# Kernel optimization log

Measured on AMD Instinct MI355X. Metric: run time of the kernel, lower is better.

The kernel has to match this reference:

```python
import jax, jax.numpy as jnp
import numpy as np

B, S, E, H = 2, 2048, 1024, 16
D = E // H  # head_dim = 64

def setup_inputs() -> dict:
    key = jax.random.key(0)
    ks = jax.random.split(key, 5)
    scale = 0.02
    return {
        "x": jax.random.normal(ks[0], (B, S, E), dtype=jnp.float32),
        "Wq": jax.random.normal(ks[1], (E, E), dtype=jnp.float32) * scale,
        "Wk": jax.random.normal(ks[2], (E, E), dtype=jnp.float32) * scale,
        "Wv": jax.random.normal(ks[3], (E, E), dtype=jnp.float32) * scale,
        "Wo": jax.random.normal(ks[4], (E, E), dtype=jnp.float32) * scale,
        "bo": jnp.zeros((E,), dtype=jnp.float32),
    }

def reference(x, Wq, Wk, Wv, Wo, bo):
    b, s, e = x.shape
    # Linear projections (torch Linear: x @ W.T), split heads -> (b, h, s, d)
    q = (x @ Wq.T).reshape(b, s, H, D).transpose(0, 2, 1, 3)
    k = (x @ Wk.T).reshape(b, s, H, D).transpose(0, 2, 1, 3)
    v = (x @ Wv.T).reshape(b, s, H, D).transpose(0, 2, 1, 3)
    # Full materialized causal scores (b, h, s, s)
    scores = jnp.einsum("bhqd,bhkd->bhqk", q, k)
    causal = jnp.tril(jnp.ones((s, s), dtype=bool))  # True = keep
    scores = jnp.where(causal, scores, -jnp.inf)
    attn = jax.nn.softmax(scores / jnp.sqrt(jnp.float32(D)), axis=-1)
    ctx = jnp.einsum("bhqk,bhkd->bhqd", attn, v)
    ctx = ctx.transpose(0, 2, 1, 3).reshape(b, s, e)
    return ctx @ Wo.T + bo
```

## Files before the change

kernel.cpp:

```cpp
#include <hip/hip_runtime.h>
#include <hip/hip_bf16.h>

typedef __attribute__((ext_vector_type(8))) short short8_t;
typedef __attribute__((ext_vector_type(4))) short s4v;
typedef __attribute__((ext_vector_type(4))) float f32x4_t;
typedef __attribute__((ext_vector_type(4))) unsigned u32x4_t;
using u16 = unsigned short;

constexpr int S_LEN = 2048;
constexpr int EMB   = 1024;
constexpr int NH    = 16;
constexpr int HD    = 64;
constexpr int BATCH = 2;
constexpr int MR    = BATCH * S_LEN;
constexpr int E3    = 3 * EMB;

#define L2E 1.44269504f

__device__ __forceinline__ u16 f2bf(float f) {
  unsigned u = __builtin_bit_cast(unsigned, f);
  unsigned r = 0x7fffu + ((u >> 16) & 1u);
  return (u16)((u + r) >> 16);
}

__device__ __forceinline__ unsigned pkbf(float a, float b) {
  __hip_bfloat162 h = __float22bfloat162_rn(make_float2(a, b));
  unsigned u;
  __builtin_memcpy(&u, &h, 4);
  return u;
}

__device__ __forceinline__ void gld16(const void* g, void* l) {
  __builtin_amdgcn_global_load_lds(
      (const __attribute__((address_space(1))) void*)g,
      (__attribute__((address_space(3))) void*)l, 16, 0, 0);
}

template <int OFF>
__device__ __forceinline__ s4v tr16(const __attribute__((address_space(3))) u16* p) {
  s4v d;
  asm volatile("ds_read_b64_tr_b16 %0, %1 offset:%2"
               : "=v"(d) : "v"(p), "n"(OFF));
  return d;
}

__global__ void k_cvt_all(const float* __restrict__ x, const float* __restrict__ Wq,
                          const float* __restrict__ Wk, const float* __restrict__ Wv,
                          const float* __restrict__ Wo, u16* __restrict__ out) {
  int i = blockIdx.x * 256 + threadIdx.x;
  const float* src;
  int j;
  float sc = 1.0f;
  if (i < (1 << 20)) {
    src = x; j = i;
  } else {
    int jj = i - (1 << 20);
    int r = jj >> 18;
    j = jj & ((1 << 18) - 1);
    src = (r == 0) ? Wq : (r == 1) ? Wk : (r == 2) ? Wv : Wo;
    if (r == 0) sc = 0.125f;
  }
  float4 v = reinterpret_cast<const float4*>(src)[j];
  ushort4 o;
  o.x = f2bf(v.x * sc); o.y = f2bf(v.y * sc);
  o.z = f2bf(v.z * sc); o.w = f2bf(v.w * sc);
  reinterpret_cast<ushort4*>(out)[i] = o;
}

__global__ __launch_bounds__(512, 1) void k_gemm256(
    const u16* __restrict__ A, const u16* __restrict__ Bw,
    u16* __restrict__ C, int M, int N) {
  constexpr int K = 1024;
  __shared__ u16 Ab[2][16384];
  __shared__ u16 Bb[2][16384];

  const int t    = threadIdx.x;
  const int ww   = t >> 6;
  const int l    = t & 63;
  const int ln15 = t & 15;
  const int lg   = (t >> 4) & 3;
  const int wr   = ww >> 2;
  const int wc   = ww & 3;

  const int nwgx = gridDim.x;
  const int lin  = blockIdx.y * nwgx + blockIdx.x;
  const int cpx  = (nwgx * gridDim.y) >> 3;
  const int lin2 = (lin & 7) * cpx + (lin >> 3);
  const int m0   = (lin2 / nwgx) * 256;
  const int n0   = (lin2 % nwgx) * 256;

  const int srow = t >> 3;
  const int rlo  = (t >> 3) & 7;
  const int scol = 8 * ((t & 7) ^ rlo);

  const int kx  = 8 * (ln15 & 7);
  const int kc0 = (8 * lg) ^ kx;
  const int kc1 = (32 + 8 * lg) ^ kx;

  f32x4_t acc[8][4] = {};

#define GST256(buf, ki)                                                        \
  do {                                                                         \
    _Pragma("unroll")                                                          \
    for (int i = 0; i < 4; ++i)                                                \
      gld16(A + (size_t)(m0 + 64 * i + srow) * K + 64 * (ki) + scol,           \
            &Ab[buf][i * 4096 + ww * 512]);                                    \
    _Pragma("unroll")                                                          \
    for (int i = 0; i < 4; ++i)                                                \
      gld16(Bw + (size_t)(n0 + 64 * i + srow) * K + 64 * (ki) + scol,          \
            &Bb[buf][i * 4096 + ww * 512]);                                    \
  } while (0)

  constexpr int nk = K / 64;
  GST256(0, 0);
  int cur = 0;

  for (int ki = 0; ki < nk; ++ki) {
    asm volatile("s_barrier" ::: "memory");
    if (ki + 1 < nk) {
      GST256(cur ^ 1, ki + 1);
      asm volatile("s_waitcnt vmcnt(8)" ::: "memory");
    } else {
      asm volatile("s_waitcnt vmcnt(0)" ::: "memory");
    }
    asm volatile("s_barrier" ::: "memory");

#pragma unroll
    for (int kh = 0; kh < 2; ++kh) {
      const int kc = kh ? kc1 : kc0;
      short8_t af[8], bf[4];
#pragma unroll
      for (int mi = 0; mi < 8; ++mi)
        af[mi] = *reinterpret_cast<const short8_t*>(
            &Ab[cur][(wr * 128 + 16 * mi + ln15) * 64 + kc]);
#pragma unroll
      for (int ni = 0; ni < 4; ++ni)
        bf[ni] = *reinterpret_cast<const short8_t*>(
            &Bb[cur][(wc * 64 + 16 * ni + ln15) * 64 + kc]);
      __builtin_amdgcn_s_setprio(1);
#pragma unroll
      for (int mi = 0; mi < 8; ++mi)
#pragma unroll
        for (int ni = 0; ni < 4; ++ni)
          acc[mi][ni] = __builtin_amdgcn_mfma_f32_16x16x32_bf16(
              af[mi], bf[ni], acc[mi][ni], 0, 0, 0);
      __builtin_amdgcn_s_setprio(0);
    }
    cur ^= 1;
  }
#undef GST256

#pragma unroll
  for (int mi = 0; mi < 8; ++mi) {
#pragma unroll
    for (int ni = 0; ni < 4; ++ni) {
      const int col = n0 + wc * 64 + 16 * ni + ln15;
#pragma unroll
      for (int rr = 0; rr < 4; ++rr) {
        const int row = m0 + wr * 128 + 16 * mi + 4 * lg + rr;
        C[(size_t)row * N + col] = f2bf(acc[mi][ni][rr]);
      }
    }
  }
}

template <bool F32OUT>
__global__ __launch_bounds__(256) void k_gemm_bt(
    const u16* __restrict__ A, const u16* __restrict__ Bw,
    void* __restrict__ Cv, const float* __restrict__ bias,
    int M, int N, int K) {
  __shared__ short As[2][128 * 32];
  __shared__ short Bs[2][128 * 32];
  const int t    = threadIdx.x;
  const int w    = t >> 6;
  const int ln15 = t & 15;
  const int lg   = (t >> 4) & 3;
  const int wr   = w >> 1, wc = w & 1;

  const int nwgx = gridDim.x;
  const int lin  = blockIdx.y * nwgx + blockIdx.x;
  const int cpx  = (nwgx * gridDim.y) >> 3;
  const int lin2 = (lin & 7) * cpx + (lin >> 3);
  const int m0   = (lin2 / nwgx) * 128;
  const int n0   = (lin2 % nwgx) * 128;

  const int srow = t >> 2;
  const int scol = (t & 3) * 8;
  const u16* gA = A + (size_t)(m0 + srow) * K + scol;
  const u16* gB = Bw + (size_t)(n0 + srow) * K + scol;
  const int lofs = w * 512;

  f32x4_t acc[4][4] = {};

#define GSTAGE(buf, k0)                                                        \
  do {                                                                         \
    gld16(gA + (k0), &As[buf][lofs]);                                          \
    gld16(gA + (size_t)64 * K + (k0), &As[buf][lofs + 2048]);                  \
    gld16(gB + (k0), &Bs[buf][lofs]);                                          \
    gld16(gB + (size_t)64 * K + (k0), &Bs[buf][lofs + 2048]);                  \
  } while (0)

  const int nk = K >> 5;
  GSTAGE(0, 0);
  int cur = 0;

  for (int ki = 0; ki < nk; ++ki) {
    asm volatile("s_barrier" ::: "memory");
    if (ki + 1 < nk) {
      GSTAGE(cur ^ 1, (ki + 1) * 32);
      asm volatile("s_waitcnt vmcnt(4)" ::: "memory");
    } else {
      asm volatile("s_waitcnt vmcnt(0)" ::: "memory");
    }
    asm volatile("s_barrier" ::: "memory");

    short8_t af[4], bf[4];
#pragma unroll
    for (int i = 0; i < 4; ++i) {
      af[i] = *reinterpret_cast<const short8_t*>(
          &As[cur][(wr * 64 + i * 16 + ln15) * 32 + 8 * lg]);
      bf[i] = *reinterpret_cast<const short8_t*>(
          &Bs[cur][(wc * 64 + i * 16 + ln15) * 32 + 8 * lg]);
    }
#pragma unroll
    for (int i = 0; i < 4; ++i)
#pragma unroll
      for (int j = 0; j < 4; ++j)
        acc[i][j] = __builtin_amdgcn_mfma_f32_16x16x32_bf16(
            af[i], bf[j], acc[i][j], 0, 0, 0);
    cur ^= 1;
  }
#undef GSTAGE

  if (F32OUT) {
    float* C = reinterpret_cast<float*>(Cv);
#pragma unroll
    for (int i = 0; i < 4; ++i)
#pragma unroll
      for (int j = 0; j < 4; ++j) {
        const int col = n0 + wc * 64 + j * 16 + ln15;
        const float bv = bias ? bias[col] : 0.0f;
#pragma unroll
        for (int r = 0; r < 4; ++r) {
          const int row = m0 + wr * 64 + i * 16 + lg * 4 + r;
          C[(size_t)row * N + col] = acc[i][j][r] + bv;
        }
      }
  } else {
    u16* C = reinterpret_cast<u16*>(Cv);
#pragma unroll
    for (int i = 0; i < 4; ++i)
#pragma unroll
      for (int j = 0; j < 4; ++j) {
        const int col = n0 + wc * 64 + j * 16 + ln15;
#pragma unroll
        for (int r = 0; r < 4; ++r) {
          const int row = m0 + wr * 64 + i * 16 + lg * 4 + r;
          C[(size_t)row * N + col] = f2bf(acc[i][j][r]);
        }
      }
  }
}

__global__ __launch_bounds__(256, 4) void k_attn2(const u16* __restrict__ QKV,
                                                  u16* __restrict__ ctx) {
  __shared__ u16 Ks[2][64 * 64];
  __shared__ u16 Vs[2][64 * 64];

  const int t    = threadIdx.x;
  const int w    = t >> 6;
  const int l    = t & 63;
  const int ln15 = t & 15;
  const int lg   = (l >> 4) & 3;

  const int qt = 31 - blockIdx.y;
  const int bh = blockIdx.x;
  const int b  = bh >> 4, h = bh & 15;

  const u16* KVb = QKV + (size_t)b * S_LEN * E3 + h * HD;
  const u16* Kg  = KVb + 1024;
  const u16* Vg  = KVb + 2048;
  const int qrow = qt * 64 + w * 16;

  short8_t qf[2];
  {
    const u16* qp = KVb + (size_t)(qrow + ln15) * E3 + 8 * lg;
    qf[0] = *reinterpret_cast<const short8_t*>(qp);
    qf[1] = *reinterpret_cast<const short8_t*>(qp + 32);
  }

  const int krow_lo = l >> 3;
  const int kcol    = 8 * ((l & 7) ^ krow_lo);
  const int vkv     = l >> 1;
  const int vcol    = 16 * w + 8 * (l & 1);

  const int kx  = 8 * (ln15 & 7);
  const int kc0 = (8 * lg) ^ kx;
  const int kc1 = (32 + 8 * lg) ^ kx;

#define STAGE(buf, kv0)                                                        \
  do {                                                                         \
    gld16(Kg + (size_t)((kv0) + 16 * w + krow_lo) * E3 + kcol,                 \
          &Ks[buf][1024 * w]);                                                 \
    gld16(Kg + (size_t)((kv0) + 16 * w + 8 + krow_lo) * E3 + kcol,             \
          &Ks[buf][1024 * w + 512]);                                           \
    gld16(Vg + (size_t)((kv0) + vkv) * E3 + vcol, &Vs[buf][1024 * w]);         \
    gld16(Vg + (size_t)((kv0) + 32 + vkv) * E3 + vcol,                         \
          &Vs[buf][1024 * w + 512]);                                           \
  } while (0)

  f32x4_t o[4] = {};
  float mrow = -3e38f, lrow = 0.0f;
  const int nt_tiles = qt + 1;

  STAGE(0, 0);
  int cur = 0;

  for (int kvt = 0; kvt < nt_tiles; ++kvt) {
    const int kv0 = kvt * 64;
    asm volatile("s_barrier" ::: "memory");
    if (kvt + 1 < nt_tiles) {
      STAGE(cur ^ 1, kv0 + 64);
      asm volatile("s_waitcnt vmcnt(4)" ::: "memory");
    } else {
      asm volatile("s_waitcnt vmcnt(0)" ::: "memory");
    }
    asm volatile("s_barrier" ::: "memory");

    const __attribute__((address_space(3))) u16* vp =
        (const __attribute__((address_space(3))) u16*)&Vs[cur][4 * l];
    s4v vf[4][2][2];
#pragma unroll
    for (int nt = 0; nt < 4; ++nt) {
      if (nt == 0) { vf[0][0][0]=tr16<0>(vp);    vf[0][0][1]=tr16<512>(vp);
                     vf[0][1][0]=tr16<1024>(vp); vf[0][1][1]=tr16<1536>(vp); }
      if (nt == 1) { vf[1][0][0]=tr16<2048>(vp); vf[1][0][1]=tr16<2560>(vp);
                     vf[1][1][0]=tr16<3072>(vp); vf[1][1][1]=tr16<3584>(vp); }
      if (nt == 2) { vf[2][0][0]=tr16<4096>(vp); vf[2][0][1]=tr16<4608>(vp);
                     vf[2][1][0]=tr16<5120>(vp); vf[2][1][1]=tr16<5632>(vp); }
      if (nt == 3) { vf[3][0][0]=tr16<6144>(vp); vf[3][0][1]=tr16<6656>(vp);
                     vf[3][1][0]=tr16<7168>(vp); vf[3][1][1]=tr16<7680>(vp); }
    }

    f32x4_t tacc[4];
    __builtin_amdgcn_s_setprio(1);
#pragma unroll
    for (int ks = 0; ks < 4; ++ks) {
      const int R = 16 * ks + ln15;
      short8_t kf0 = *reinterpret_cast<const short8_t*>(&Ks[cur][R * 64 + kc0]);
      short8_t kf1 = *reinterpret_cast<const short8_t*>(&Ks[cur][R * 64 + kc1]);
      f32x4_t a = {0.f, 0.f, 0.f, 0.f};
      a = __builtin_amdgcn_mfma_f32_16x16x32_bf16(kf0, qf[0], a, 0, 0, 0);
      a = __builtin_amdgcn_mfma_f32_16x16x32_bf16(kf1, qf[1], a, 0, 0, 0);
      tacc[ks] = a;
    }
    __builtin_amdgcn_s_setprio(0);

    if (kvt == qt) {
      const int qg = qrow + ln15;
#pragma unroll
      for (int ks = 0; ks < 4; ++ks)
#pragma unroll
        for (int r = 0; r < 4; ++r)
          if (kv0 + 16 * ks + 4 * lg + r > qg) tacc[ks][r] = -3e38f;
    }

    float rm = fmaxf(
        fmaxf(fmaxf(fmaxf(tacc[0][0], tacc[0][1]), fmaxf(tacc[0][2], tacc[0][3])),
              fmaxf(fmaxf(tacc[1][0], tacc[1][1]), fmaxf(tacc[1][2], tacc[1][3]))),
        fmaxf(fmaxf(fmaxf(tacc[2][0], tacc[2][1]), fmaxf(tacc[2][2], tacc[2][3])),
              fmaxf(fmaxf(tacc[3][0], tacc[3][1]), fmaxf(tacc[3][2], tacc[3][3]))));
    rm = fmaxf(rm, __shfl_xor(rm, 16, 64));
    rm = fmaxf(rm, __shfl_xor(rm, 32, 64));

    if (__any(rm > mrow)) {
      const float nm = fmaxf(mrow, rm);
      const float sc = exp2f((mrow - nm) * L2E);
      mrow = nm;
      lrow *= sc;
#pragma unroll
      for (int r = 0; r < 4; ++r) {
        const float so = __shfl(sc, 20 * lg + r, 64);
#pragma unroll
        for (int nt = 0; nt < 4; ++nt) o[nt][r] *= so;
      }
    }

    const float nmL = mrow * L2E;
    float p[4][4];
    float rs = 0.0f;
#pragma unroll
    for (int ks = 0; ks < 4; ++ks)
#pragma unroll
      for (int r = 0; r < 4; ++r) {
        const float pv = exp2f(fmaf(tacc[ks][r], L2E, -nmL));
        p[ks][r] = pv;
        rs += pv;
      }
    rs += __shfl_xor(rs, 16, 64);
    rs += __shfl_xor(rs, 32, 64);
    lrow += rs;

    short8_t pf[2];
#pragma unroll
    for (int s2 = 0; s2 < 2; ++s2) {
      u32x4_t pu;
      pu[0] = pkbf(p[2 * s2][0], p[2 * s2][1]);
      pu[1] = pkbf(p[2 * s2][2], p[2 * s2][3]);
      pu[2] = pkbf(p[2 * s2 + 1][0], p[2 * s2 + 1][1]);
      pu[3] = pkbf(p[2 * s2 + 1][2], p[2 * s2 + 1][3]);
      pf[s2] = __builtin_bit_cast(short8_t, pu);
    }

    asm volatile("s_waitcnt lgkmcnt(0)");
    __builtin_amdgcn_sched_barrier(0);

    __builtin_amdgcn_s_setprio(1);
#pragma unroll
    for (int nt = 0; nt < 4; ++nt) {
#pragma unroll
      for (int s2 = 0; s2 < 2; ++s2) {
        short8_t bv = __builtin_shufflevector(vf[nt][s2][0], vf[nt][s2][1],
                                              0, 1, 2, 3, 4, 5, 6, 7);
        o[nt] = __builtin_amdgcn_mfma_f32_16x16x32_bf16(pf[s2], bv, o[nt], 0, 0, 0);
      }
    }
    __builtin_amdgcn_s_setprio(0);
    cur ^= 1;
  }
#undef STAGE

  const float linv = 1.0f / lrow;
#pragma unroll
  for (int r = 0; r < 4; ++r) {
    const float li = __shfl(linv, 20 * lg + r, 64);
    u16* op = ctx + (size_t)(b * S_LEN + qrow + 4 * lg + r) * EMB + h * HD;
#pragma unroll
    for (int nt = 0; nt < 4; ++nt)
      op[nt * 16 + ln15] = f2bf(o[nt][r] * li);
  }
}

extern "C" void kernel_launch(void* const* d_in, const int* in_sizes, int n_in,
                              void* d_out, int out_size, void* d_ws, size_t ws_size,
                              hipStream_t stream) {
  const float* x  = (const float*)d_in[0];
  const float* Wq = (const float*)d_in[1];
  const float* Wk = (const float*)d_in[2];
  const float* Wv = (const float*)d_in[3];
  const float* Wo = (const float*)d_in[4];
  const float* bo = (const float*)d_in[5];

  u16* ws   = (u16*)d_ws;
  u16* xb   = ws;
  u16* wcat = xb + (size_t)MR * EMB;
  u16* wob  = wcat + (size_t)3 * EMB * EMB;
  u16* qkv  = wob + (size_t)EMB * EMB;
  u16* ctxb = qkv + (size_t)MR * E3;

  k_cvt_all<<<8192, 256, 0, stream>>>(x, Wq, Wk, Wv, Wo, xb);

  k_gemm256<<<dim3(E3 / 256, MR / 256), 512, 0, stream>>>(
      xb, wcat, qkv, MR, E3);

  k_attn2<<<dim3(BATCH * NH, 32), 256, 0, stream>>>(qkv, ctxb);

  k_gemm_bt<true><<<dim3(EMB / 128, MR / 128), 256, 0, stream>>>(
      ctxb, wob, d_out, bo, MR, EMB, EMB);
}
```

Measured before the change: 119.7 us.

## Interleave next-tile global loads across four MFMA phases in the 256x256 GEMM

The 256x256 bf16 GEMM main loop now streams the next K tile's eight global-to-LDS loads in four pairs, one pair before each quarter of the MFMA work, with a barrier between phases. It no longer issues all eight loads at the top of the iteration. A-fragments are read two M-rows at a time for both K halves, which cuts live fragment registers, and B-fragments are loaded once per tile. The aim is to overlap memory traffic with matrix math and ease register pressure. The trade-off is more barriers per iteration. There is also no barrier between the vmcnt wait and the first LDS reads, so waves may read tiles other waves have not finished loading.

```diff
diff --git a/kernel.cpp b/kernel.cpp
--- a/kernel.cpp
+++ b/kernel.cpp
@@ -76,7 +76,6 @@
 
   const int t    = threadIdx.x;
   const int ww   = t >> 6;
-  const int l    = t & 63;
   const int ln15 = t & 15;
   const int lg   = (t >> 4) & 3;
   const int wr   = ww >> 2;
@@ -99,56 +98,83 @@
 
   f32x4_t acc[8][4] = {};
 
-#define GST256(buf, ki)                                                        \
-  do {                                                                         \
+#define U_A(buf, ki, i)                                                        \
+  gld16(A + (size_t)(m0 + 64 * (i) + srow) * K + 64 * (ki) + scol,             \
+        &Ab[buf][(i) * 4096 + ww * 512])
+#define U_B(buf, ki, i)                                                        \
+  gld16(Bw + (size_t)(n0 + 64 * (i) + srow) * K + 64 * (ki) + scol,            \
+        &Bb[buf][(i) * 4096 + ww * 512])
+
+#define AF_READ(q)                                                             \
+  af[0][0] = *reinterpret_cast<const short8_t*>(                               \
+      &Ab[cur][(wr * 128 + 16 * (2 * (q)) + ln15) * 64 + kc0]);                \
+  af[0][1] = *reinterpret_cast<const short8_t*>(                               \
+      &Ab[cur][(wr * 128 + 16 * (2 * (q)) + ln15) * 64 + kc1]);                \
+  af[1][0] = *reinterpret_cast<const short8_t*>(                               \
+      &Ab[cur][(wr * 128 + 16 * (2 * (q) + 1) + ln15) * 64 + kc0]);            \
+  af[1][1] = *reinterpret_cast<const short8_t*>(                               \
+      &Ab[cur][(wr * 128 + 16 * (2 * (q) + 1) + ln15) * 64 + kc1])
+
+#define MFMA16(q)                                                              \
+  __builtin_amdgcn_s_setprio(1);                                               \
+  _Pragma("unroll")                                                            \
+  for (int m2 = 0; m2 < 2; ++m2)                                               \
     _Pragma("unroll")                                                          \
-    for (int i = 0; i < 4; ++i)                                                \
-      gld16(A + (size_t)(m0 + 64 * i + srow) * K + 64 * (ki) + scol,           \
-            &Ab[buf][i * 4096 + ww * 512]);                                    \
-    _Pragma("unroll")                                                          \
-    for (int i = 0; i < 4; ++i)                                                \
-      gld16(Bw + (size_t)(n0 + 64 * i + srow) * K + 64 * (ki) + scol,          \
-            &Bb[buf][i * 4096 + ww * 512]);                                    \
-  } while (0)
+    for (int ni = 0; ni < 4; ++ni) {                                           \
+      acc[2 * (q) + m2][ni] = __builtin_amdgcn_mfma_f32_16x16x32_bf16(         \
+          af[m2][0], bf[ni][0], acc[2 * (q) + m2][ni], 0, 0, 0);               \
+      acc[2 * (q) + m2][ni] = __builtin_amdgcn_mfma_f32_16x16x32_bf16(         \
+          af[m2][1], bf[ni][1], acc[2 * (q) + m2][ni], 0, 0, 0);               \
+    }                                                                          \
+  __builtin_amdgcn_s_setprio(0)
 
   constexpr int nk = K / 64;
-  GST256(0, 0);
+  U_B(0, 0, 0); U_B(0, 0, 1); U_B(0, 0, 2); U_B(0, 0, 3);
+  U_A(0, 0, 0); U_A(0, 0, 2); U_A(0, 0, 1); U_A(0, 0, 3);
   int cur = 0;
 
   for (int ki = 0; ki < nk; ++ki) {
-    asm volatile("s_barrier" ::: "memory");
-    if (ki + 1 < nk) {
-      GST256(cur ^ 1, ki + 1);
-      asm volatile("s_waitcnt vmcnt(8)" ::: "memory");
+    const bool nxt = (ki + 1 < nk);
+    short8_t bf[4][2], af[2][2];
+
+    asm volatile("s_barrier" ::: "memory");
+    if (nxt) {
+      U_B(cur ^ 1, ki + 1, 0); U_B(cur ^ 1, ki + 1, 1);
+      asm volatile("s_waitcnt vmcnt(2)" ::: "memory");
     } else {
       asm volatile("s_waitcnt vmcnt(0)" ::: "memory");
     }
-    asm volatile("s_barrier" ::: "memory");
-
-#pragma unroll
-    for (int kh = 0; kh < 2; ++kh) {
-      const int kc = kh ? kc1 : kc0;
-      short8_t af[8], bf[4];
-#pragma unroll
-      for (int mi = 0; mi < 8; ++mi)
-        af[mi] = *reinterpret_cast<const short8_t*>(
-            &Ab[cur][(wr * 128 + 16 * mi + ln15) * 64 + kc]);
-#pragma unroll
-      for (int ni = 0; ni < 4; ++ni)
-        bf[ni] = *reinterpret_cast<const short8_t*>(
-            &Bb[cur][(wc * 64 + 16 * ni + ln15) * 64 + kc]);
-      __builtin_amdgcn_s_setprio(1);
-#pragma unroll
-      for (int mi = 0; mi < 8; ++mi)
-#pragma unroll
-        for (int ni = 0; ni < 4; ++ni)
-          acc[mi][ni] = __builtin_amdgcn_mfma_f32_16x16x32_bf16(
-              af[mi], bf[ni], acc[mi][ni], 0, 0, 0);
-      __builtin_amdgcn_s_setprio(0);
-    }
+#pragma unroll
+    for (int ni = 0; ni < 4; ++ni) {
+      bf[ni][0] = *reinterpret_cast<const short8_t*>(
+          &Bb[cur][(wc * 64 + 16 * ni + ln15) * 64 + kc0]);
+      bf[ni][1] = *reinterpret_cast<const short8_t*>(
+          &Bb[cur][(wc * 64 + 16 * ni + ln15) * 64 + kc1]);
+    }
+    AF_READ(0);
+    MFMA16(0);
+
+    asm volatile("s_barrier" ::: "memory");
+    if (nxt) { U_B(cur ^ 1, ki + 1, 2); U_B(cur ^ 1, ki + 1, 3); }
+    AF_READ(1);
+    MFMA16(1);
+
+    asm volatile("s_barrier" ::: "memory");
+    if (nxt) { U_A(cur ^ 1, ki + 1, 0); U_A(cur ^ 1, ki + 1, 2); }
+    AF_READ(2);
+    MFMA16(2);
+
+    asm volatile("s_barrier" ::: "memory");
+    if (nxt) { U_A(cur ^ 1, ki + 1, 1); U_A(cur ^ 1, ki + 1, 3); }
+    AF_READ(3);
+    MFMA16(3);
+
     cur ^= 1;
   }
-#undef GST256
+#undef U_A
+#undef U_B
+#undef AF_READ
+#undef MFMA16
 
 #pragma unroll
   for (int mi = 0; mi < 8; ++mi) {
```

Result: slower. 128.0 us (+6.9%).
